# Optimization experiments

Hardware: AMD Instinct MI355X
Metric: run time of the kernel (lower is better)

## Reference

```python
import jax, jax.numpy as jnp
import numpy as np

N_ENTITY = 200000
N_WORD = 30001  # word_num + 1 (last row = padding)
EMBED = 64
HEADS = 4
HEAD_DIM = EMBED // HEADS
CONV_NUM = 3
N_EDGES = 6_400_000
BATCH = 1024
Q_LEN = 20
N_NEG = 5


def setup_inputs() -> dict:
    key = jax.random.key(0)
    ks = jax.random.split(key, 14)
    entity_w = jax.random.normal(ks[0], (N_ENTITY, EMBED), jnp.float32) * 0.02
    word_w = jax.random.normal(ks[1], (N_WORD, EMBED), jnp.float32) * 0.02
    word_w = word_w.at[N_WORD - 1].set(0.0)  # padding_idx row
    in_proj_w = jax.random.normal(ks[2], (3 * EMBED, EMBED), jnp.float32) * 0.05
    in_proj_b = jnp.zeros((3 * EMBED,), jnp.float32)
    out_proj_w = jax.random.normal(ks[3], (EMBED, EMBED), jnp.float32) * 0.05
    out_proj_b = jnp.zeros((EMBED,), jnp.float32)
    edge_row = jax.random.randint(ks[4], (N_EDGES,), 0, N_ENTITY, jnp.int32)
    edge_col = jax.random.randint(ks[5], (N_EDGES,), 0, N_ENTITY, jnp.int32)
    # symmetric-normalized adjacency values ~ 1/sqrt(deg_i*deg_j); avg degree 32 -> ~1/32
    edge_val = jax.random.uniform(ks[6], (N_EDGES,), jnp.float32) * (1.0 / 16.0)
    users = jax.random.randint(ks[7], (BATCH,), 0, N_ENTITY, jnp.int32)
    items = jax.random.randint(ks[8], (BATCH,), 0, N_ENTITY, jnp.int32)
    query_words = jax.random.randint(ks[9], (BATCH, Q_LEN), 0, N_WORD - 1, jnp.int32)
    neg_items = jax.random.randint(ks[10], (BATCH, N_NEG), 0, N_ENTITY, jnp.int32)
    return dict(entity_w=entity_w, word_w=word_w, in_proj_w=in_proj_w,
                in_proj_b=in_proj_b, out_proj_w=out_proj_w, out_proj_b=out_proj_b,
                edge_val=edge_val, users=users, items=items,
                query_words=query_words, neg_items=neg_items,
                edge_row=edge_row, edge_col=edge_col)


def _graph_update(entity_w, edge_row, edge_col, edge_val):
    # LightGCN-style: mean over layer-0..conv_num embeddings of repeated SpMM
    h = entity_w
    acc = entity_w
    for _ in range(CONV_NUM):
        h = jax.ops.segment_sum(edge_val[:, None] * h[edge_col], edge_row,
                                num_segments=N_ENTITY)  # [N, E]
        acc = acc + h
    return acc / (CONV_NUM + 1)


def _sent_encode(query_words, word_w, in_proj_w, in_proj_b, out_proj_w, out_proj_b):
    x = word_w[query_words]                                  # [B, Q, E]
    qkv = x @ in_proj_w.T + in_proj_b                        # [B, Q, 3E]
    q, k, v = jnp.split(qkv, 3, axis=-1)
    B, Q = x.shape[0], x.shape[1]
    q = q.reshape(B, Q, HEADS, HEAD_DIM)
    k = k.reshape(B, Q, HEADS, HEAD_DIM)
    v = v.reshape(B, Q, HEADS, HEAD_DIM)
    scores = jnp.einsum('bqhd,bkhd->bhqk', q, k) / jnp.sqrt(jnp.float32(HEAD_DIM))
    attn = jax.nn.softmax(scores, axis=-1)
    ctx = jnp.einsum('bhqk,bkhd->bqhd', attn, v).reshape(B, Q, EMBED)
    out = ctx @ out_proj_w.T + out_proj_b                    # [B, Q, E]
    return out.mean(axis=1)                                  # [B, E]


def _triplet_match_loss(u, pos, neg):
    # BPR-style: -log sigmoid(<u,pos> - <u,neg>)
    s_pos = jnp.sum(u * pos, axis=-1)                        # [B]
    s_neg = jnp.einsum('bd,bnd->bn', u, neg)                 # [B, n]
    return -jax.nn.log_sigmoid(s_pos[:, None] - s_neg).mean()


def _nce_loss(p, pos, neg):
    s_pos = jnp.sum(p * pos, axis=-1)                        # [B]
    s_neg = jnp.einsum('bd,bnd->bn', p, neg)                 # [B, n]
    return (-jax.nn.log_sigmoid(s_pos)).mean() + (-jax.nn.log_sigmoid(-s_neg)).mean()


def reference(entity_w, word_w, in_proj_w, in_proj_b, out_proj_w, out_proj_b,
              edge_val, users, items, query_words, neg_items,
              edge_row, edge_col):
    graph = _graph_update(entity_w, edge_row, edge_col, edge_val)
    query_encode = _sent_encode(query_words, word_w, in_proj_w, in_proj_b,
                                out_proj_w, out_proj_b)
    user_embed = graph[users]
    personalized = query_encode + 0.1 * user_embed
    item_embed = graph[items]
    neg_item_embed = graph[neg_items]
    cf_loss = _triplet_match_loss(user_embed, item_embed, neg_item_embed)
    search_loss = _nce_loss(personalized, item_embed, neg_item_embed)
    return search_loss + cf_loss
```

## Files before the change

kernel.cpp:

```cpp
#include <hip/hip_runtime.h>
#include <math.h>

#define N_ENTITY 200000
#define EMBED    64
#define N_EDGES  6400000
#define BATCH    1024
#define QLEN     20
#define NNEG     5
#define NSEL     (BATCH + BATCH + BATCH*NNEG)
#define BM_WORDS ((N_ENTITY + 31) / 32)
#define COLMASK  0x3FFFF

#define BROWS     512
#define ROWSH     9
#define NBUCKET   ((N_ENTITY + BROWS - 1) / BROWS)
#define NBLK_PART 512

typedef unsigned int   uint32;
typedef unsigned short ushort16;

__device__ __forceinline__ ushort16 f2bf(float f) {
    uint32 b = __float_as_uint(f);
    uint32 r = (b + 0x7FFFu + ((b >> 16) & 1u)) >> 16;
    return (ushort16)r;
}
__device__ __forceinline__ float bf2f(ushort16 h) {
    return __uint_as_float(((uint32)h) << 16);
}
__device__ __forceinline__ float bflo(uint32 p) { return __uint_as_float(p << 16); }
__device__ __forceinline__ float bfhi(uint32 p) { return __uint_as_float(p & 0xFFFF0000u); }
__device__ __forceinline__ float edgev(int y) { return __uint_as_float(((uint32)y & 0xFFFFu) << 16); }

__device__ __forceinline__ int sel_row(int i, const int* users, const int* items,
                                       const int* negs) {
    if (i < BATCH)        return users[i];
    if (i < 2 * BATCH)    return items[i - BATCH];
    return negs[i - 2 * BATCH];
}

__global__ void part_hist_kernel(const int* __restrict__ erow,
                                 int* __restrict__ bucket_cnt,
                                 int* __restrict__ blockBase) {
    __shared__ int h[NBUCKET];
    int blk = blockIdx.x, t = threadIdx.x;
    for (int i = t; i < NBUCKET; i += 256) h[i] = 0;
    __syncthreads();
    int per = (N_EDGES + NBLK_PART - 1) / NBLK_PART;
    int s = blk * per, e = min(s + per, N_EDGES);
    for (int j = s + t; j < e; j += 256)
        atomicAdd(&h[erow[j] >> ROWSH], 1);
    __syncthreads();
    for (int i = t; i < NBUCKET; i += 256)
        blockBase[blk * NBUCKET + i] = atomicAdd(&bucket_cnt[i], h[i]);
}

__global__ void bucket_scan_kernel(const int* __restrict__ cnt,
                                   int* __restrict__ bstart) {
    __shared__ int s[256];
    int t = threadIdx.x;
    int i0 = t * 2, i1 = t * 2 + 1;
    int c0 = (i0 < NBUCKET) ? cnt[i0] : 0;
    int c1 = (i1 < NBUCKET) ? cnt[i1] : 0;
    s[t] = c0 + c1; __syncthreads();
    for (int off = 1; off < 256; off <<= 1) {
        int x = (t >= off) ? s[t - off] : 0;
        __syncthreads();
        s[t] += x;
        __syncthreads();
    }
    int excl = t ? s[t - 1] : 0;
    if (i0 <= NBUCKET) { if (i0 < NBUCKET) bstart[i0] = excl; else bstart[NBUCKET] = excl; }
    excl += c0;
    if (i1 <= NBUCKET) { if (i1 < NBUCKET) bstart[i1] = excl; else bstart[NBUCKET] = excl; }
    if (t == 255) bstart[NBUCKET] = s[255];
}

__global__ void part_scatter_kernel(const int* __restrict__ erow,
                                    const int* __restrict__ ecol,
                                    const float* __restrict__ evalv,
                                    const int* __restrict__ bstart,
                                    const int* __restrict__ blockBase,
                                    int2* __restrict__ ebuf) {
    __shared__ int cur[NBUCKET];
    int blk = blockIdx.x, t = threadIdx.x;
    for (int i = t; i < NBUCKET; i += 256)
        cur[i] = bstart[i] + blockBase[blk * NBUCKET + i];
    __syncthreads();
    int per = (N_EDGES + NBLK_PART - 1) / NBLK_PART;
    int s = blk * per, e = min(s + per, N_EDGES);
    int j = s + t;
    for (; j + 256 < e; j += 512) {
        int   r0 = erow[j],       r1 = erow[j + 256];
        int   c0 = ecol[j],       c1 = ecol[j + 256];
        float v0 = evalv[j],      v1 = evalv[j + 256];
        int p0 = atomicAdd(&cur[r0 >> ROWSH], 1);
        int p1 = atomicAdd(&cur[r1 >> ROWSH], 1);
        ebuf[p0] = make_int2(c0 | ((r0 & (BROWS-1)) << 18), (int)f2bf(v0));
        ebuf[p1] = make_int2(c1 | ((r1 & (BROWS-1)) << 18), (int)f2bf(v1));
    }
    for (; j < e; j += 256) {
        int   r = erow[j];
        int   c = ecol[j];
        float v = evalv[j];
        int pos = atomicAdd(&cur[r >> ROWSH], 1);
        ebuf[pos] = make_int2(c | ((r & (BROWS-1)) << 18), (int)f2bf(v));
    }
}

__global__ void bucket_sort_kernel(const int2* __restrict__ ebuf,
                                   const int* __restrict__ bstart,
                                   int2* __restrict__ ebuf2,
                                   int* __restrict__ rowptr) {
    __shared__ int cur[BROWS];
    int b = blockIdx.x, t = threadIdx.x;
    int beg = bstart[b], end = bstart[b + 1];
    cur[t] = 0;
    __syncthreads();
    for (int j = beg + t; j < end; j += BROWS)
        atomicAdd(&cur[((unsigned)ebuf[j].x) >> 18], 1);
    __syncthreads();
    int own = cur[t];
    __syncthreads();
    cur[t] = own;
    __syncthreads();
    for (int off = 1; off < BROWS; off <<= 1) {
        int x = (t >= off) ? cur[t - off] : 0;
        __syncthreads();
        cur[t] += x;
        __syncthreads();
    }
    int excl = cur[t] - own;
    __syncthreads();
    int r = (b << ROWSH) + t;
    if (r <= N_ENTITY) rowptr[r] = beg + excl;
    cur[t] = beg + excl;
    __syncthreads();
    for (int j = beg + t; j < end; j += BROWS) {
        int2 e = ebuf[j];
        int pos = atomicAdd(&cur[((unsigned)e.x) >> 18], 1);
        ebuf2[pos] = e;
    }
}

__global__ void need_build_kernel(const int* __restrict__ users,
                                  const int* __restrict__ items,
                                  const int* __restrict__ negs,
                                  const int* __restrict__ rowptr,
                                  const int2* __restrict__ edges,
                                  unsigned int* __restrict__ bm) {
    int lane = threadIdx.x & 63;
    int wave = blockIdx.x * (blockDim.x >> 6) + (threadIdx.x >> 6);
    if (wave >= NSEL) return;
    int idx = sel_row(wave, users, items, negs);
    if (lane == 0) atomicOr(&bm[idx >> 5], 1u << (idx & 31));
    int beg = rowptr[idx], end = rowptr[idx + 1];
    for (int j = beg + lane; j < end; j += 64) {
        int c = edges[j].x & COLMASK;
        atomicOr(&bm[c >> 5], 1u << (c & 31));
    }
}

__global__ void conv_bf16_kernel(const float* __restrict__ src,
                                 ushort16* __restrict__ dst) {
    int i = (blockIdx.x * blockDim.x + threadIdx.x) * 4;
    if (i >= N_ENTITY * EMBED) return;
    float4 v = *(const float4*)&src[i];
    uint32 p0 = (uint32)f2bf(v.x) | ((uint32)f2bf(v.y) << 16);
    uint32 p1 = (uint32)f2bf(v.z) | ((uint32)f2bf(v.w) << 16);
    *(uint2*)&dst[i] = make_uint2(p0, p1);
}

template<int FILTER>
__global__ void spmm_bf16_kernel(const ushort16* __restrict__ src,
                                 ushort16* __restrict__ dst,
                                 const int* __restrict__ rowptr,
                                 const int2* __restrict__ edges,
                                 const unsigned int* __restrict__ bm) {
    int lane = threadIdx.x & 63;
    int half = lane >> 5;
    int l2   = lane & 31;
    int wave  = blockIdx.x * (blockDim.x >> 6) + (threadIdx.x >> 6);
    int nwave = gridDim.x * (blockDim.x >> 6);
    for (int row = wave; row < N_ENTITY; row += nwave) {
        if (FILTER && !((bm[row >> 5] >> (row & 31)) & 1u)) continue;
        int beg = rowptr[row], end = rowptr[row + 1];
        int cnt = end - beg;
        int h0  = cnt - (cnt >> 1);
        int s   = beg + half * h0;
        int e   = half ? end : (beg + h0);
        float ax = 0.f, ay = 0.f;
        int j = s;
        for (; j + 7 < e; j += 8) {
            int2 e0 = edges[j],   e1 = edges[j+1], e2 = edges[j+2], e3 = edges[j+3];
            int2 e4 = edges[j+4], e5 = edges[j+5], e6 = edges[j+6], e7 = edges[j+7];
            uint32 p0 = *(const uint32*)&src[(size_t)(e0.x & COLMASK) * EMBED + l2 * 2];
            uint32 p1 = *(const uint32*)&src[(size_t)(e1.x & COLMASK) * EMBED + l2 * 2];
            uint32 p2 = *(const uint32*)&src[(size_t)(e2.x & COLMASK) * EMBED + l2 * 2];
            uint32 p3 = *(const uint32*)&src[(size_t)(e3.x & COLMASK) * EMBED + l2 * 2];
            uint32 p4 = *(const uint32*)&src[(size_t)(e4.x & COLMASK) * EMBED + l2 * 2];
            uint32 p5 = *(const uint32*)&src[(size_t)(e5.x & COLMASK) * EMBED + l2 * 2];
            uint32 p6 = *(const uint32*)&src[(size_t)(e6.x & COLMASK) * EMBED + l2 * 2];
            uint32 p7 = *(const uint32*)&src[(size_t)(e7.x & COLMASK) * EMBED + l2 * 2];
            float v0 = edgev(e0.y), v1 = edgev(e1.y), v2 = edgev(e2.y), v3 = edgev(e3.y);
            float v4 = edgev(e4.y), v5 = edgev(e5.y), v6 = edgev(e6.y), v7 = edgev(e7.y);
            ax += v0 * bflo(p0);  ay += v0 * bfhi(p0);
            ax += v1 * bflo(p1);  ay += v1 * bfhi(p1);
            ax += v2 * bflo(p2);  ay += v2 * bfhi(p2);
            ax += v3 * bflo(p3);  ay += v3 * bfhi(p3);
            ax += v4 * bflo(p4);  ay += v4 * bfhi(p4);
            ax += v5 * bflo(p5);  ay += v5 * bfhi(p5);
            ax += v6 * bflo(p6);  ay += v6 * bfhi(p6);
            ax += v7 * bflo(p7);  ay += v7 * bfhi(p7);
        }
        for (; j + 3 < e; j += 4) {
            int2 e0 = edges[j], e1 = edges[j+1], e2 = edges[j+2], e3 = edges[j+3];
            uint32 p0 = *(const uint32*)&src[(size_t)(e0.x & COLMASK) * EMBED + l2 * 2];
            uint32 p1 = *(const uint32*)&src[(size_t)(e1.x & COLMASK) * EMBED + l2 * 2];
            uint32 p2 = *(const uint32*)&src[(size_t)(e2.x & COLMASK) * EMBED + l2 * 2];
            uint32 p3 = *(const uint32*)&src[(size_t)(e3.x & COLMASK) * EMBED + l2 * 2];
            float v0 = edgev(e0.y), v1 = edgev(e1.y), v2 = edgev(e2.y), v3 = edgev(e3.y);
            ax += v0 * bflo(p0);  ay += v0 * bfhi(p0);
            ax += v1 * bflo(p1);  ay += v1 * bfhi(p1);
            ax += v2 * bflo(p2);  ay += v2 * bfhi(p2);
            ax += v3 * bflo(p3);  ay += v3 * bfhi(p3);
        }
        for (; j < e; ++j) {
            int2 ed = edges[j];
            float v = edgev(ed.y);
            uint32 p = *(const uint32*)&src[(size_t)(ed.x & COLMASK) * EMBED + l2 * 2];
            ax += v * bflo(p);
            ay += v * bfhi(p);
        }
        ax += __shfl_xor(ax, 32);
        ay += __shfl_xor(ay, 32);
        if (half == 0) {
            uint32 packed = (uint32)f2bf(ax) | ((uint32)f2bf(ay) << 16);
            *(uint32*)&dst[(size_t)row * EMBED + l2 * 2] = packed;
        }
    }
}

__global__ void sel_pull_kernel(const ushort16* __restrict__ h,
                                const int* __restrict__ users,
                                const int* __restrict__ items,
                                const int* __restrict__ negs,
                                const int* __restrict__ rowptr,
                                const int2* __restrict__ edges,
                                float* __restrict__ sel) {
    int lane = threadIdx.x & 63;
    int wave = blockIdx.x * (blockDim.x >> 6) + (threadIdx.x >> 6);
    if (wave >= NSEL) return;
    int idx = sel_row(wave, users, items, negs);
    int beg = rowptr[idx], end = rowptr[idx + 1];
    float acc = 0.f;
    int j = beg;
    for (; j + 7 < end; j += 8) {
        int2 e0 = edges[j],   e1 = edges[j+1], e2 = edges[j+2], e3 = edges[j+3];
        int2 e4 = edges[j+4], e5 = edges[j+5], e6 = edges[j+6], e7 = edges[j+7];
        float x0 = bf2f(h[(size_t)(e0.x & COLMASK) * EMBED + lane]);
        float x1 = bf2f(h[(size_t)(e1.x & COLMASK) * EMBED + lane]);
        float x2 = bf2f(h[(size_t)(e2.x & COLMASK) * EMBED + lane]);
        float x3 = bf2f(h[(size_t)(e3.x & COLMASK) * EMBED + lane]);
        float x4 = bf2f(h[(size_t)(e4.x & COLMASK) * EMBED + lane]);
        float x5 = bf2f(h[(size_t)(e5.x & COLMASK) * EMBED + lane]);
        float x6 = bf2f(h[(size_t)(e6.x & COLMASK) * EMBED + lane]);
        float x7 = bf2f(h[(size_t)(e7.x & COLMASK) * EMBED + lane]);
        acc += edgev(e0.y) * x0;
        acc += edgev(e1.y) * x1;
        acc += edgev(e2.y) * x2;
        acc += edgev(e3.y) * x3;
        acc += edgev(e4.y) * x4;
        acc += edgev(e5.y) * x5;
        acc += edgev(e6.y) * x6;
        acc += edgev(e7.y) * x7;
    }
    for (; j < end; ++j) {
        int2 e = edges[j];
        acc += edgev(e.y) * bf2f(h[(size_t)(e.x & COLMASK) * EMBED + lane]);
    }
    sel[(size_t)wave * EMBED + lane] += acc;
}

__global__ void sel_init_kernel(const float* __restrict__ h,
                                const int* __restrict__ users,
                                const int* __restrict__ items,
                                const int* __restrict__ negs,
                                float* __restrict__ sel) {
    int tid = blockIdx.x * blockDim.x + threadIdx.x;
    if (tid >= NSEL * EMBED) return;
    int i = tid >> 6, d = tid & 63;
    int idx = sel_row(i, users, items, negs);
    sel[tid] = h[(size_t)idx * EMBED + d];
}

__global__ void sel_add_bf16_kernel(const ushort16* __restrict__ h,
                                    const int* __restrict__ users,
                                    const int* __restrict__ items,
                                    const int* __restrict__ negs,
                                    float* __restrict__ sel) {
    int tid = blockIdx.x * blockDim.x + threadIdx.x;
    if (tid >= NSEL * EMBED) return;
    int i = tid >> 6, d = tid & 63;
    int idx = sel_row(i, users, items, negs);
    sel[tid] += bf2f(h[(size_t)idx * EMBED + d]);
}

__global__ void qkv_kernel(const int* __restrict__ qwords,
                           const float* __restrict__ word_w,
                           const float* __restrict__ Win,
                           const float* __restrict__ bin,
                           float* __restrict__ qkv_g) {
    __shared__ float Wl[192][65];
    __shared__ float xw[QLEN][65];
    __shared__ float bl[192];
    int b = blockIdx.x, t = threadIdx.x;

    for (int j = t; j < 192 * EMBED; j += 256) {
        int o = j >> 6, d = j & 63;
        Wl[o][d] = Win[j];
    }
    for (int j = t; j < 192; j += 256) bl[j] = bin[j];
    for (int j = t; j < QLEN * EMBED; j += 256) {
        int q = j >> 6, d = j & 63;
        int w = qwords[b * QLEN + q];
        xw[q][d] = word_w[(size_t)w * EMBED + d];
    }
    __syncthreads();

    for (int j = t; j < QLEN * 192; j += 256) {
        int q = j / 192, o = j % 192;
        float acc = bl[o];
        #pragma unroll
        for (int d = 0; d < EMBED; ++d) acc += xw[q][d] * Wl[o][d];
        qkv_g[(size_t)b * QLEN * 192 + j] = acc;
    }
}

__global__ void attn_kernel(const float* __restrict__ qkv_g,
                            const float* __restrict__ Wout,
                            const float* __restrict__ bout,
                            float* __restrict__ qenc) {
    __shared__ float qs[QLEN][195];
    __shared__ float ctx[QLEN][68];
    __shared__ float Wl[64][65];
    __shared__ float mctx[EMBED];
    int b = blockIdx.x, t = threadIdx.x;

    for (int j = t; j < QLEN * 192; j += 128) {
        int q = j / 192, o = j % 192;
        qs[q][o] = qkv_g[(size_t)b * QLEN * 192 + j];
    }
    for (int j = t; j < EMBED * EMBED; j += 128) {
        int o = j >> 6, d = j & 63;
        Wl[o][d] = Wout[j];
    }
    __syncthreads();

    if (t < 4 * QLEN) {
        int h = t / QLEN, i = t % QLEN;
        float sc[QLEN];
        float mx = -1e30f;
        #pragma unroll
        for (int k = 0; k < QLEN; ++k) {
            float s = 0.f;
            #pragma unroll
            for (int d = 0; d < 16; ++d)
                s += qs[i][h*16 + d] * qs[k][EMBED + h*16 + d];
            s *= 0.25f;
            sc[k] = s;
            mx = fmaxf(mx, s);
        }
        float denom = 0.f;
        #pragma unroll
        for (int k = 0; k < QLEN; ++k) { sc[k] = expf(sc[k] - mx); denom += sc[k]; }
        float inv = 1.0f / denom;
        #pragma unroll
        for (int d = 0; d < 16; ++d) {
            float acc = 0.f;
            #pragma unroll
            for (int k = 0; k < QLEN; ++k)
                acc += sc[k] * qs[k][2*EMBED + h*16 + d];
            ctx[i][h*16 + d] = acc * inv;
        }
    }
    __syncthreads();

    if (t < EMBED) {
        float acc = 0.f;
        #pragma unroll
        for (int q = 0; q < QLEN; ++q) acc += ctx[q][t];
        mctx[t] = acc * (1.0f / QLEN);
    }
    __syncthreads();

    if (t < EMBED) {
        float acc = bout[t];
        #pragma unroll
        for (int d = 0; d < EMBED; ++d) acc += mctx[d] * Wl[t][d];
        qenc[b * EMBED + t] = acc;
    }
}

__global__ void spmm_kernel(const float* __restrict__ src, float* __restrict__ dst,
                            const int* __restrict__ erow, const int* __restrict__ ecol,
                            const float* __restrict__ evalv, int n_edges) {
    int lane  = threadIdx.x & 63;
    int wave  = blockIdx.x * (blockDim.x >> 6) + (threadIdx.x >> 6);
    int nwave = gridDim.x * (blockDim.x >> 6);
    for (int e = wave; e < n_edges; e += nwave) {
        int   r = erow[e];
        int   c = ecol[e];
        float v = evalv[e];
        float x = src[(size_t)c * EMBED + lane];
        atomicAdd(&dst[(size_t)r * EMBED + lane], v * x);
    }
}

__global__ void spmm_filtered_kernel(const float* __restrict__ src, float* __restrict__ dst,
                                     const int* __restrict__ erow, const int* __restrict__ ecol,
                                     const float* __restrict__ evalv,
                                     const unsigned int* __restrict__ bm, int n_edges) {
    int lane  = threadIdx.x & 63;
    int wave  = blockIdx.x * (blockDim.x >> 6) + (threadIdx.x >> 6);
    int nwave = gridDim.x * (blockDim.x >> 6);
    for (int e = wave; e < n_edges; e += nwave) {
        int r = erow[e];
        if (!((bm[r >> 5] >> (r & 31)) & 1u)) continue;
        int   c = ecol[e];
        float v = evalv[e];
        float x = src[(size_t)c * EMBED + lane];
        atomicAdd(&dst[(size_t)r * EMBED + lane], v * x);
    }
}

__global__ void bitmap_build_kernel(const int* __restrict__ users,
                                    const int* __restrict__ items,
                                    const int* __restrict__ negs,
                                    unsigned int* __restrict__ bm) {
    int i = blockIdx.x * blockDim.x + threadIdx.x;
    if (i >= NSEL) return;
    int idx = sel_row(i, users, items, negs);
    atomicOr(&bm[idx >> 5], 1u << (idx & 31));
}

__global__ void sel_accum_kernel(const float* __restrict__ h,
                                 const int* __restrict__ users,
                                 const int* __restrict__ items,
                                 const int* __restrict__ negs,
                                 float* __restrict__ sel, int init) {
    int tid = blockIdx.x * blockDim.x + threadIdx.x;
    if (tid >= NSEL * EMBED) return;
    int i = tid >> 6, d = tid & 63;
    int idx = sel_row(i, users, items, negs);
    float v = h[(size_t)idx * EMBED + d];
    if (init) sel[tid] = v;
    else      sel[tid] += v;
}

__global__ void sent_kernel(const int* __restrict__ qwords,
                            const float* __restrict__ word_w,
                            const float* __restrict__ Win,  const float* __restrict__ bin,
                            const float* __restrict__ Wout, const float* __restrict__ bout,
                            float* __restrict__ qenc) {
    __shared__ float x[QLEN][EMBED];
    __shared__ float qkv[QLEN][3*EMBED];
    __shared__ float ctx[QLEN][EMBED];
    __shared__ float mctx[EMBED];
    int b = blockIdx.x;
    int t = threadIdx.x;

    for (int j = t; j < QLEN*EMBED; j += 128) {
        int q = j >> 6, d = j & 63;
        int w = qwords[b*QLEN + q];
        x[q][d] = word_w[(size_t)w * EMBED + d];
    }
    __syncthreads();
    for (int j = t; j < QLEN*192; j += 128) {
        int q = j / 192, o = j % 192;
        float acc = bin[o];
        const float* wrow = &Win[o*EMBED];
        #pragma unroll
        for (int d = 0; d < EMBED; ++d) acc += x[q][d] * wrow[d];
        qkv[q][o] = acc;
    }
    __syncthreads();
    if (t < 4*QLEN) {
        int h = t / QLEN, i = t % QLEN;
        float sc[QLEN];
        float mx = -1e30f;
        #pragma unroll
        for (int k = 0; k < QLEN; ++k) {
            float s = 0.f;
            #pragma unroll
            for (int d = 0; d < 16; ++d)
                s += qkv[i][h*16 + d] * qkv[k][EMBED + h*16 + d];
            s *= 0.25f;
            sc[k] = s;
            mx = fmaxf(mx, s);
        }
        float denom = 0.f;
        #pragma unroll
        for (int k = 0; k < QLEN; ++k) { sc[k] = expf(sc[k] - mx); denom += sc[k]; }
        float inv = 1.0f / denom;
        #pragma unroll
        for (int d = 0; d < 16; ++d) {
            float acc = 0.f;
            #pragma unroll
            for (int k = 0; k < QLEN; ++k)
                acc += sc[k] * qkv[k][2*EMBED + h*16 + d];
            ctx[i][h*16 + d] = acc * inv;
        }
    }
    __syncthreads();
    if (t < EMBED) {
        float acc = 0.f;
        #pragma unroll
        for (int q = 0; q < QLEN; ++q) acc += ctx[q][t];
        mctx[t] = acc * (1.0f/QLEN);
    }
    __syncthreads();
    if (t < EMBED) {
        float acc = bout[t];
        const float* wrow = &Wout[t*EMBED];
        #pragma unroll
        for (int d = 0; d < EMBED; ++d) acc += mctx[d] * wrow[d];
        qenc[b*EMBED + t] = acc;
    }
}

__device__ __forceinline__ float log_sigmoid(float x) {
    float l = log1pf(expf(-fabsf(x)));
    return x >= 0.f ? -l : x - l;
}
__device__ __forceinline__ float wred(float v) {
    #pragma unroll
    for (int off = 32; off; off >>= 1) v += __shfl_xor(v, off);
    return v;
}

__global__ void loss_kernel(const float* __restrict__ sel,
                            const float* __restrict__ qenc,
                            float* __restrict__ out) {
    int b = blockIdx.x;
    int d = threadIdx.x;
    const float scale = 0.25f;
    float u   = sel[(size_t)b*EMBED + d] * scale;
    float pos = sel[(size_t)(BATCH + b)*EMBED + d] * scale;
    float p   = qenc[b*EMBED + d] + 0.1f * u;

    float s_up = wred(u * pos);
    float s_pp = wred(p * pos);
    float nu[NNEG], np_[NNEG];
    #pragma unroll
    for (int n = 0; n < NNEG; ++n) {
        float ng = sel[(size_t)(2*BATCH + b*NNEG + n)*EMBED + d] * scale;
        nu[n]  = wred(u * ng);
        np_[n] = wred(p * ng);
    }
    if (d == 0) {
        float cf = 0.f, srch_neg = 0.f;
        #pragma unroll
        for (int n = 0; n < NNEG; ++n) {
            cf       += -log_sigmoid(s_up - nu[n]);
            srch_neg += -log_sigmoid(-np_[n]);
        }
        float res = cf * (1.0f/(BATCH*NNEG))
                  + (-log_sigmoid(s_pp)) * (1.0f/BATCH)
                  + srch_neg * (1.0f/(BATCH*NNEG));
        atomicAdd(out, res);
    }
}

extern "C" void kernel_launch(void* const* d_in, const int* in_sizes, int n_in,
                              void* d_out, int out_size, void* d_ws, size_t ws_size,
                              hipStream_t stream) {
    const float* entity_w   = (const float*)d_in[0];
    const float* word_w     = (const float*)d_in[1];
    const float* in_proj_w  = (const float*)d_in[2];
    const float* in_proj_b  = (const float*)d_in[3];
    const float* out_proj_w = (const float*)d_in[4];
    const float* out_proj_b = (const float*)d_in[5];
    const float* edge_val   = (const float*)d_in[6];
    const int*   users      = (const int*)d_in[7];
    const int*   items      = (const int*)d_in[8];
    const int*   qwords     = (const int*)d_in[9];
    const int*   neg_items  = (const int*)d_in[10];
    const int*   edge_row   = (const int*)d_in[11];
    const int*   edge_col   = (const int*)d_in[12];
    float* out = (float*)d_out;

    const size_t HN  = (size_t)N_ENTITY * EMBED;
    const size_t HNB = HN * sizeof(ushort16);
    const size_t EB  = sizeof(int2) * (size_t)N_EDGES;
    const size_t QKVN = (size_t)BATCH * QLEN * 192;

    size_t need = EB
                + EB
                + HNB
                + sizeof(float) * (size_t)NSEL * EMBED
                + sizeof(float) * (size_t)BATCH * EMBED
                + sizeof(int) * (size_t)(N_ENTITY + 1)
                + sizeof(unsigned int) * (size_t)BM_WORDS
                + sizeof(float) * QKVN;

    hipMemsetAsync(out, 0, sizeof(float) * out_size, stream);

    if (ws_size >= need) {
        char* base = (char*)d_ws;
        int2*      ebuf2 = (int2*)base;
        int2*      ebuf  = (int2*)(base + EB);
        ushort16*  e16   = (ushort16*)(base + EB);
        ushort16*  h1    = (ushort16*)(base + EB + HNB);
        char* p = base + 2 * EB;
        ushort16*  h2    = (ushort16*)p;     p += HNB;
        float*     sel   = (float*)p;        p += sizeof(float) * (size_t)NSEL * EMBED;
        float*     qenc  = (float*)p;        p += sizeof(float) * (size_t)BATCH * EMBED;
        int*       rowptr = (int*)p;         p += sizeof(int) * (size_t)(N_ENTITY + 1);
        unsigned int* bmNeed = (unsigned int*)p;  p += sizeof(unsigned int) * (size_t)BM_WORDS;
        float*     qkv_g = (float*)p;
        int* bucket_cnt = (int*)h2;
        int* bstart     = bucket_cnt + NBUCKET;
        int* blockBase  = bstart + NBUCKET + 1;

        hipMemsetAsync(bucket_cnt, 0, sizeof(int) * NBUCKET, stream);
        hipMemsetAsync(bmNeed, 0, sizeof(unsigned int) * BM_WORDS, stream);

        part_hist_kernel<<<NBLK_PART, 256, 0, stream>>>(edge_row, bucket_cnt, blockBase);
        bucket_scan_kernel<<<1, 256, 0, stream>>>(bucket_cnt, bstart);
        part_scatter_kernel<<<NBLK_PART, 256, 0, stream>>>(
            edge_row, edge_col, edge_val, bstart, blockBase, ebuf);
        bucket_sort_kernel<<<NBUCKET, BROWS, 0, stream>>>(ebuf, bstart, ebuf2, rowptr);

        need_build_kernel<<<(NSEL + 3) / 4, 256, 0, stream>>>(
            users, items, neg_items, rowptr, ebuf2, bmNeed);

        qkv_kernel<<<BATCH, 256, 0, stream>>>(qwords, word_w, in_proj_w, in_proj_b, qkv_g);
        attn_kernel<<<BATCH, 128, 0, stream>>>(qkv_g, out_proj_w, out_proj_b, qenc);

        conv_bf16_kernel<<<(N_ENTITY * EMBED / 4 + 255) / 256, 256, 0, stream>>>(
            entity_w, e16);

        sel_init_kernel<<<(NSEL * EMBED) / 256, 256, 0, stream>>>(
            entity_w, users, items, neg_items, sel);

        spmm_bf16_kernel<0><<<2048, 256, 0, stream>>>(e16, h1, rowptr, ebuf2, nullptr);
        sel_add_bf16_kernel<<<(NSEL * EMBED) / 256, 256, 0, stream>>>(
            h1, users, items, neg_items, sel);

        spmm_bf16_kernel<1><<<2048, 256, 0, stream>>>(h1, h2, rowptr, ebuf2, bmNeed);
        sel_add_bf16_kernel<<<(NSEL * EMBED) / 256, 256, 0, stream>>>(
            h2, users, items, neg_items, sel);

        sel_pull_kernel<<<(NSEL + 3) / 4, 256, 0, stream>>>(
            h2, users, items, neg_items, rowptr, ebuf2, sel);

        loss_kernel<<<BATCH, 64, 0, stream>>>(sel, qenc, out);
    } else {
        float* hA   = (float*)d_ws;
        float* hB   = hA + HN;
        float* sel  = hB + HN;
        float* qenc = sel + (size_t)NSEL * EMBED;
        unsigned int* bm = (unsigned int*)(qenc + (size_t)BATCH * EMBED);

        hipMemsetAsync(bm, 0, sizeof(unsigned int) * BM_WORDS, stream);
        bitmap_build_kernel<<<(NSEL + 255) / 256, 256, 0, stream>>>(users, items, neg_items, bm);
        sel_accum_kernel<<<(NSEL * EMBED) / 256, 256, 0, stream>>>(
            entity_w, users, items, neg_items, sel, 1);
        hipMemsetAsync(hA, 0, HN * sizeof(float), stream);
        spmm_kernel<<<2048, 256, 0, stream>>>(entity_w, hA, edge_row, edge_col, edge_val, N_EDGES);
        sel_accum_kernel<<<(NSEL * EMBED) / 256, 256, 0, stream>>>(
            hA, users, items, neg_items, sel, 0);
        hipMemsetAsync(hB, 0, HN * sizeof(float), stream);
        spmm_kernel<<<2048, 256, 0, stream>>>(hA, hB, edge_row, edge_col, edge_val, N_EDGES);
        sel_accum_kernel<<<(NSEL * EMBED) / 256, 256, 0, stream>>>(
            hB, users, items, neg_items, sel, 0);
        hipMemsetAsync(hA, 0, HN * sizeof(float), stream);
        spmm_filtered_kernel<<<2048, 256, 0, stream>>>(hB, hA, edge_row, edge_col, edge_val, bm, N_EDGES);
        sel_accum_kernel<<<(NSEL * EMBED) / 256, 256, 0, stream>>>(
            hA, users, items, neg_items, sel, 0);
        sent_kernel<<<BATCH, 128, 0, stream>>>(qwords, word_w, in_proj_w, in_proj_b,
                                               out_proj_w, out_proj_b, qenc);
        loss_kernel<<<BATCH, 64, 0, stream>>>(sel, qenc, out);
    }
}
```

Before: 557.1 us.

## Pack edges into 32-bit words, gather quarter-rows, and compact filtered rows

The sorted edge list is stored as one 32-bit word per edge: an 18-bit column index plus a truncated bf16 value in the upper bits. This halves the edge bytes streamed by the SpMM and pull kernels. The SpMM now splits each row across four 16-lane groups, each loading 8 bytes per neighbor and fetching edge words with vector int4 loads. A new kernel turns the need-bitmap into a compact row list, so the filtered second SpMM no longer scans all rows. The cost is less precision in edge values, since two mantissa bits are dropped, and possibly misaligned int4 loads.

```diff
diff --git a/kernel.cpp b/kernel.cpp
--- a/kernel.cpp
+++ b/kernel.cpp
@@ -10,6 +10,7 @@
 #define NSEL     (BATCH + BATCH + BATCH*NNEG)
 #define BM_WORDS ((N_ENTITY + 31) / 32)
 #define COLMASK  0x3FFFF
+#define VALMASK  0xFFFC0000u
 
 #define BROWS     512
 #define ROWSH     9
@@ -29,7 +30,7 @@
 }
 __device__ __forceinline__ float bflo(uint32 p) { return __uint_as_float(p << 16); }
 __device__ __forceinline__ float bfhi(uint32 p) { return __uint_as_float(p & 0xFFFF0000u); }
-__device__ __forceinline__ float edgev(int y) { return __uint_as_float(((uint32)y & 0xFFFFu) << 16); }
+__device__ __forceinline__ float pval(uint32 p) { return __uint_as_float(p & VALMASK); }
 
 __device__ __forceinline__ int sel_row(int i, const int* users, const int* items,
                                        const int* negs) {
@@ -109,7 +110,7 @@
 
 __global__ void bucket_sort_kernel(const int2* __restrict__ ebuf,
                                    const int* __restrict__ bstart,
-                                   int2* __restrict__ ebuf2,
+                                   int* __restrict__ epack,
                                    int* __restrict__ rowptr) {
     __shared__ int cur[BROWS];
     int b = blockIdx.x, t = threadIdx.x;
@@ -138,7 +139,7 @@
     for (int j = beg + t; j < end; j += BROWS) {
         int2 e = ebuf[j];
         int pos = atomicAdd(&cur[((unsigned)e.x) >> 18], 1);
-        ebuf2[pos] = e;
+        epack[pos] = (e.x & COLMASK) | ((e.y & 0xFFFC) << 16);
     }
 }
 
@@ -146,7 +147,7 @@
                                   const int* __restrict__ items,
                                   const int* __restrict__ negs,
                                   const int* __restrict__ rowptr,
-                                  const int2* __restrict__ edges,
+                                  const int* __restrict__ epack,
                                   unsigned int* __restrict__ bm) {
     int lane = threadIdx.x & 63;
     int wave = blockIdx.x * (blockDim.x >> 6) + (threadIdx.x >> 6);
@@ -155,8 +156,24 @@
     if (lane == 0) atomicOr(&bm[idx >> 5], 1u << (idx & 31));
     int beg = rowptr[idx], end = rowptr[idx + 1];
     for (int j = beg + lane; j < end; j += 64) {
-        int c = edges[j].x & COLMASK;
+        int c = epack[j] & COLMASK;
         atomicOr(&bm[c >> 5], 1u << (c & 31));
+    }
+}
+
+__global__ void list_build_kernel(const unsigned int* __restrict__ bm,
+                                  int* __restrict__ rowlist,
+                                  int* __restrict__ nrow) {
+    int w = blockIdx.x * blockDim.x + threadIdx.x;
+    if (w >= BM_WORDS) return;
+    unsigned int m = bm[w];
+    if (!m) return;
+    int n = __popc(m);
+    int base = atomicAdd(nrow, n);
+    while (m) {
+        int b = __ffs(m) - 1;
+        m &= m - 1;
+        rowlist[base++] = (w << 5) + b;
     }
 }
 
@@ -170,72 +187,65 @@
     *(uint2*)&dst[i] = make_uint2(p0, p1);
 }
 
-template<int FILTER>
-__global__ void spmm_bf16_kernel(const ushort16* __restrict__ src,
-                                 ushort16* __restrict__ dst,
-                                 const int* __restrict__ rowptr,
-                                 const int2* __restrict__ edges,
-                                 const unsigned int* __restrict__ bm) {
+template<int USELIST>
+__global__ void spmm_q_kernel(const ushort16* __restrict__ src,
+                              ushort16* __restrict__ dst,
+                              const int* __restrict__ rowptr,
+                              const int* __restrict__ epack,
+                              const int* __restrict__ rowlist,
+                              const int* __restrict__ nrowp) {
     int lane = threadIdx.x & 63;
-    int half = lane >> 5;
-    int l2   = lane & 31;
+    int qt   = lane >> 4;
+    int l4   = lane & 15;
     int wave  = blockIdx.x * (blockDim.x >> 6) + (threadIdx.x >> 6);
     int nwave = gridDim.x * (blockDim.x >> 6);
-    for (int row = wave; row < N_ENTITY; row += nwave) {
-        if (FILTER && !((bm[row >> 5] >> (row & 31)) & 1u)) continue;
+    int nrow = USELIST ? *nrowp : N_ENTITY;
+    for (int it = wave; it < nrow; it += nwave) {
+        int row = USELIST ? rowlist[it] : it;
         int beg = rowptr[row], end = rowptr[row + 1];
         int cnt = end - beg;
-        int h0  = cnt - (cnt >> 1);
-        int s   = beg + half * h0;
-        int e   = half ? end : (beg + h0);
-        float ax = 0.f, ay = 0.f;
+        int qn  = (cnt + 3) >> 2;
+        int s   = beg + qt * qn;
+        int e   = min(s + qn, end);
+        float a0 = 0.f, a1 = 0.f, a2 = 0.f, a3 = 0.f;
         int j = s;
         for (; j + 7 < e; j += 8) {
-            int2 e0 = edges[j],   e1 = edges[j+1], e2 = edges[j+2], e3 = edges[j+3];
-            int2 e4 = edges[j+4], e5 = edges[j+5], e6 = edges[j+6], e7 = edges[j+7];
-            uint32 p0 = *(const uint32*)&src[(size_t)(e0.x & COLMASK) * EMBED + l2 * 2];
-            uint32 p1 = *(const uint32*)&src[(size_t)(e1.x & COLMASK) * EMBED + l2 * 2];
-            uint32 p2 = *(const uint32*)&src[(size_t)(e2.x & COLMASK) * EMBED + l2 * 2];
-            uint32 p3 = *(const uint32*)&src[(size_t)(e3.x & COLMASK) * EMBED + l2 * 2];
-            uint32 p4 = *(const uint32*)&src[(size_t)(e4.x & COLMASK) * EMBED + l2 * 2];
-            uint32 p5 = *(const uint32*)&src[(size_t)(e5.x & COLMASK) * EMBED + l2 * 2];
-            uint32 p6 = *(const uint32*)&src[(size_t)(e6.x & COLMASK) * EMBED + l2 * 2];
-            uint32 p7 = *(const uint32*)&src[(size_t)(e7.x & COLMASK) * EMBED + l2 * 2];
-            float v0 = edgev(e0.y), v1 = edgev(e1.y), v2 = edgev(e2.y), v3 = edgev(e3.y);
-            float v4 = edgev(e4.y), v5 = edgev(e5.y), v6 = edgev(e6.y), v7 = edgev(e7.y);
-            ax += v0 * bflo(p0);  ay += v0 * bfhi(p0);
-            ax += v1 * bflo(p1);  ay += v1 * bfhi(p1);
-            ax += v2 * bflo(p2);  ay += v2 * bfhi(p2);
-            ax += v3 * bflo(p3);  ay += v3 * bfhi(p3);
-            ax += v4 * bflo(p4);  ay += v4 * bfhi(p4);
-            ax += v5 * bflo(p5);  ay += v5 * bfhi(p5);
-            ax += v6 * bflo(p6);  ay += v6 * bfhi(p6);
-            ax += v7 * bflo(p7);  ay += v7 * bfhi(p7);
-        }
-        for (; j + 3 < e; j += 4) {
-            int2 e0 = edges[j], e1 = edges[j+1], e2 = edges[j+2], e3 = edges[j+3];
-            uint32 p0 = *(const uint32*)&src[(size_t)(e0.x & COLMASK) * EMBED + l2 * 2];
-            uint32 p1 = *(const uint32*)&src[(size_t)(e1.x & COLMASK) * EMBED + l2 * 2];
-            uint32 p2 = *(const uint32*)&src[(size_t)(e2.x & COLMASK) * EMBED + l2 * 2];
-            uint32 p3 = *(const uint32*)&src[(size_t)(e3.x & COLMASK) * EMBED + l2 * 2];
-            float v0 = edgev(e0.y), v1 = edgev(e1.y), v2 = edgev(e2.y), v3 = edgev(e3.y);
-            ax += v0 * bflo(p0);  ay += v0 * bfhi(p0);
-            ax += v1 * bflo(p1);  ay += v1 * bfhi(p1);
-            ax += v2 * bflo(p2);  ay += v2 * bfhi(p2);
-            ax += v3 * bflo(p3);  ay += v3 * bfhi(p3);
+            int4 ca = *(const int4*)&epack[j];
+            int4 cb = *(const int4*)&epack[j + 4];
+            uint2 p0 = *(const uint2*)&src[(size_t)(ca.x & COLMASK) * EMBED + l4 * 4];
+            uint2 p1 = *(const uint2*)&src[(size_t)(ca.y & COLMASK) * EMBED + l4 * 4];
+            uint2 p2 = *(const uint2*)&src[(size_t)(ca.z & COLMASK) * EMBED + l4 * 4];
+            uint2 p3 = *(const uint2*)&src[(size_t)(ca.w & COLMASK) * EMBED + l4 * 4];
+            uint2 p4 = *(const uint2*)&src[(size_t)(cb.x & COLMASK) * EMBED + l4 * 4];
+            uint2 p5 = *(const uint2*)&src[(size_t)(cb.y & COLMASK) * EMBED + l4 * 4];
+            uint2 p6 = *(const uint2*)&src[(size_t)(cb.z & COLMASK) * EMBED + l4 * 4];
+            uint2 p7 = *(const uint2*)&src[(size_t)(cb.w & COLMASK) * EMBED + l4 * 4];
+            float v0 = pval(ca.x), v1 = pval(ca.y), v2 = pval(ca.z), v3 = pval(ca.w);
+            float v4 = pval(cb.x), v5 = pval(cb.y), v6 = pval(cb.z), v7 = pval(cb.w);
+            a0 += v0 * bflo(p0.x); a1 += v0 * bfhi(p0.x); a2 += v0 * bflo(p0.y); a3 += v0 * bfhi(p0.y);
+            a0 += v1 * bflo(p1.x); a1 += v1 * bfhi(p1.x); a2 += v1 * bflo(p1.y); a3 += v1 * bfhi(p1.y);
+            a0 += v2 * bflo(p2.x); a1 += v2 * bfhi(p2.x); a2 += v2 * bflo(p2.y); a3 += v2 * bfhi(p2.y);
+            a0 += v3 * bflo(p3.x); a1 += v3 * bfhi(p3.x); a2 += v3 * bflo(p3.y); a3 += v3 * bfhi(p3.y);
+            a0 += v4 * bflo(p4.x); a1 += v4 * bfhi(p4.x); a2 += v4 * bflo(p4.y); a3 += v4 * bfhi(p4.y);
+            a0 += v5 * bflo(p5.x); a1 += v5 * bfhi(p5.x); a2 += v5 * bflo(p5.y); a3 += v5 * bfhi(p5.y);
+            a0 += v6 * bflo(p6.x); a1 += v6 * bfhi(p6.x); a2 += v6 * bflo(p6.y); a3 += v6 * bfhi(p6.y);
+            a0 += v7 * bflo(p7.x); a1 += v7 * bfhi(p7.x); a2 += v7 * bflo(p7.y); a3 += v7 * bfhi(p7.y);
         }
         for (; j < e; ++j) {
-            int2 ed = edges[j];
-            float v = edgev(ed.y);
-            uint32 p = *(const uint32*)&src[(size_t)(ed.x & COLMASK) * EMBED + l2 * 2];
-            ax += v * bflo(p);
-            ay += v * bfhi(p);
+            uint32 pe = (uint32)epack[j];
+            uint2 p = *(const uint2*)&src[(size_t)(pe & COLMASK) * EMBED + l4 * 4];
+            float v = pval(pe);
+            a0 += v * bflo(p.x); a1 += v * bfhi(p.x);
+            a2 += v * bflo(p.y); a3 += v * bfhi(p.y);
         }
-        ax += __shfl_xor(ax, 32);
-        ay += __shfl_xor(ay, 32);
-        if (half == 0) {
-            uint32 packed = (uint32)f2bf(ax) | ((uint32)f2bf(ay) << 16);
-            *(uint32*)&dst[(size_t)row * EMBED + l2 * 2] = packed;
+        a0 += __shfl_xor(a0, 16); a0 += __shfl_xor(a0, 32);
+        a1 += __shfl_xor(a1, 16); a1 += __shfl_xor(a1, 32);
+        a2 += __shfl_xor(a2, 16); a2 += __shfl_xor(a2, 32);
+        a3 += __shfl_xor(a3, 16); a3 += __shfl_xor(a3, 32);
+        if (qt == 0) {
+            uint32 lo = (uint32)f2bf(a0) | ((uint32)f2bf(a1) << 16);
+            uint32 hi = (uint32)f2bf(a2) | ((uint32)f2bf(a3) << 16);
+            *(uint2*)&dst[(size_t)row * EMBED + l4 * 4] = make_uint2(lo, hi);
         }
     }
 }
@@ -245,7 +255,7 @@
                                 const int* __restrict__ items,
                                 const int* __restrict__ negs,
                                 const int* __restrict__ rowptr,
-                                const int2* __restrict__ edges,
+                                const int* __restrict__ epack,
                                 float* __restrict__ sel) {
     int lane = threadIdx.x & 63;
     int wave = blockIdx.x * (blockDim.x >> 6) + (threadIdx.x >> 6);
@@ -255,28 +265,28 @@
     float acc = 0.f;
     int j = beg;
     for (; j + 7 < end; j += 8) {
-        int2 e0 = edges[j],   e1 = edges[j+1], e2 = edges[j+2], e3 = edges[j+3];
-        int2 e4 = edges[j+4], e5 = edges[j+5], e6 = edges[j+6], e7 = edges[j+7];
-        float x0 = bf2f(h[(size_t)(e0.x & COLMASK) * EMBED + lane]);
-        float x1 = bf2f(h[(size_t)(e1.x & COLMASK) * EMBED + lane]);
-        float x2 = bf2f(h[(size_t)(e2.x & COLMASK) * EMBED + lane]);
-        float x3 = bf2f(h[(size_t)(e3.x & COLMASK) * EMBED + lane]);
-        float x4 = bf2f(h[(size_t)(e4.x & COLMASK) * EMBED + lane]);
-        float x5 = bf2f(h[(size_t)(e5.x & COLMASK) * EMBED + lane]);
-        float x6 = bf2f(h[(size_t)(e6.x & COLMASK) * EMBED + lane]);
-        float x7 = bf2f(h[(size_t)(e7.x & COLMASK) * EMBED + lane]);
-        acc += edgev(e0.y) * x0;
-        acc += edgev(e1.y) * x1;
-        acc += edgev(e2.y) * x2;
-        acc += edgev(e3.y) * x3;
-        acc += edgev(e4.y) * x4;
-        acc += edgev(e5.y) * x5;
-        acc += edgev(e6.y) * x6;
-        acc += edgev(e7.y) * x7;
+        uint32 e0 = epack[j],   e1 = epack[j+1], e2 = epack[j+2], e3 = epack[j+3];
+        uint32 e4 = epack[j+4], e5 = epack[j+5], e6 = epack[j+6], e7 = epack[j+7];
+        float x0 = bf2f(h[(size_t)(e0 & COLMASK) * EMBED + lane]);
+        float x1 = bf2f(h[(size_t)(e1 & COLMASK) * EMBED + lane]);
+        float x2 = bf2f(h[(size_t)(e2 & COLMASK) * EMBED + lane]);
+        float x3 = bf2f(h[(size_t)(e3 & COLMASK) * EMBED + lane]);
+        float x4 = bf2f(h[(size_t)(e4 & COLMASK) * EMBED + lane]);
+        float x5 = bf2f(h[(size_t)(e5 & COLMASK) * EMBED + lane]);
+        float x6 = bf2f(h[(size_t)(e6 & COLMASK) * EMBED + lane]);
+        float x7 = bf2f(h[(size_t)(e7 & COLMASK) * EMBED + lane]);
+        acc += pval(e0) * x0;
+        acc += pval(e1) * x1;
+        acc += pval(e2) * x2;
+        acc += pval(e3) * x3;
+        acc += pval(e4) * x4;
+        acc += pval(e5) * x5;
+        acc += pval(e6) * x6;
+        acc += pval(e7) * x7;
     }
     for (; j < end; ++j) {
-        int2 e = edges[j];
-        acc += edgev(e.y) * bf2f(h[(size_t)(e.x & COLMASK) * EMBED + lane]);
+        uint32 e = epack[j];
+        acc += pval(e) * bf2f(h[(size_t)(e & COLMASK) * EMBED + lane]);
     }
     sel[(size_t)wave * EMBED + lane] += acc;
 }
@@ -594,45 +604,52 @@
     const size_t EB  = sizeof(int2) * (size_t)N_EDGES;
     const size_t QKVN = (size_t)BATCH * QLEN * 192;
 
-    size_t need = EB
+    size_t need = sizeof(int) * (size_t)N_EDGES
                 + EB
                 + HNB
                 + sizeof(float) * (size_t)NSEL * EMBED
                 + sizeof(float) * (size_t)BATCH * EMBED
                 + sizeof(int) * (size_t)(N_ENTITY + 1)
                 + sizeof(unsigned int) * (size_t)BM_WORDS
-                + sizeof(float) * QKVN;
+                + sizeof(float) * QKVN
+                + sizeof(int) * (size_t)N_ENTITY
+                + 64;
 
     hipMemsetAsync(out, 0, sizeof(float) * out_size, stream);
 
     if (ws_size >= need) {
         char* base = (char*)d_ws;
-        int2*      ebuf2 = (int2*)base;
-        int2*      ebuf  = (int2*)(base + EB);
-        ushort16*  e16   = (ushort16*)(base + EB);
-        ushort16*  h1    = (ushort16*)(base + EB + HNB);
-        char* p = base + 2 * EB;
+        int*       epack = (int*)base;
+        int2*      ebuf  = (int2*)(base + sizeof(int) * (size_t)N_EDGES);
+        ushort16*  e16   = (ushort16*)ebuf;
+        ushort16*  h1    = (ushort16*)((char*)ebuf + HNB);
+        char* p = (char*)ebuf + EB;
         ushort16*  h2    = (ushort16*)p;     p += HNB;
         float*     sel   = (float*)p;        p += sizeof(float) * (size_t)NSEL * EMBED;
         float*     qenc  = (float*)p;        p += sizeof(float) * (size_t)BATCH * EMBED;
         int*       rowptr = (int*)p;         p += sizeof(int) * (size_t)(N_ENTITY + 1);
         unsigned int* bmNeed = (unsigned int*)p;  p += sizeof(unsigned int) * (size_t)BM_WORDS;
-        float*     qkv_g = (float*)p;
+        float*     qkv_g = (float*)p;        p += sizeof(float) * QKVN;
+        int*       rowlist = (int*)p;        p += sizeof(int) * (size_t)N_ENTITY;
+        int*       nrow = (int*)p;
         int* bucket_cnt = (int*)h2;
         int* bstart     = bucket_cnt + NBUCKET;
         int* blockBase  = bstart + NBUCKET + 1;
 
         hipMemsetAsync(bucket_cnt, 0, sizeof(int) * NBUCKET, stream);
         hipMemsetAsync(bmNeed, 0, sizeof(unsigned int) * BM_WORDS, stream);
+        hipMemsetAsync(nrow, 0, sizeof(int), stream);
 
         part_hist_kernel<<<NBLK_PART, 256, 0, stream>>>(edge_row, bucket_cnt, blockBase);
         bucket_scan_kernel<<<1, 256, 0, stream>>>(bucket_cnt, bstart);
         part_scatter_kernel<<<NBLK_PART, 256, 0, stream>>>(
             edge_row, edge_col, edge_val, bstart, blockBase, ebuf);
-        bucket_sort_kernel<<<NBUCKET, BROWS, 0, stream>>>(ebuf, bstart, ebuf2, rowptr);
+        bucket_sort_kernel<<<NBUCKET, BROWS, 0, stream>>>(ebuf, bstart, epack, rowptr);
 
         need_build_kernel<<<(NSEL + 3) / 4, 256, 0, stream>>>(
-            users, items, neg_items, rowptr, ebuf2, bmNeed);
+            users, items, neg_items, rowptr, epack, bmNeed);
+        list_build_kernel<<<(BM_WORDS + 255) / 256, 256, 0, stream>>>(
+            bmNeed, rowlist, nrow);
 
         qkv_kernel<<<BATCH, 256, 0, stream>>>(qwords, word_w, in_proj_w, in_proj_b, qkv_g);
         attn_kernel<<<BATCH, 128, 0, stream>>>(qkv_g, out_proj_w, out_proj_b, qenc);
@@ -643,16 +660,16 @@
         sel_init_kernel<<<(NSEL * EMBED) / 256, 256, 0, stream>>>(
             entity_w, users, items, neg_items, sel);
 
-        spmm_bf16_kernel<0><<<2048, 256, 0, stream>>>(e16, h1, rowptr, ebuf2, nullptr);
+        spmm_q_kernel<0><<<2048, 256, 0, stream>>>(e16, h1, rowptr, epack, nullptr, nullptr);
         sel_add_bf16_kernel<<<(NSEL * EMBED) / 256, 256, 0, stream>>>(
             h1, users, items, neg_items, sel);
 
-        spmm_bf16_kernel<1><<<2048, 256, 0, stream>>>(h1, h2, rowptr, ebuf2, bmNeed);
+        spmm_q_kernel<1><<<2048, 256, 0, stream>>>(h1, h2, rowptr, epack, rowlist, nrow);
         sel_add_bf16_kernel<<<(NSEL * EMBED) / 256, 256, 0, stream>>>(
             h2, users, items, neg_items, sel);
 
         sel_pull_kernel<<<(NSEL + 3) / 4, 256, 0, stream>>>(
-            h2, users, items, neg_items, rowptr, ebuf2, sel);
+            h2, users, items, neg_items, rowptr, epack, sel);
 
         loss_kernel<<<BATCH, 64, 0, stream>>>(sel, qenc, out);
     } else {
```

New measurement: 557.8 us. About the same (+0.1%).
